# Kernel tuning notes

Hardware: AMD Instinct MI355X
Metric: run time of the kernel (lower is better)

## Reference

```python
import jax, jax.numpy as jnp
import numpy as np

PATCH = 7          # patch_size (stride fixed to 1, loop=False)
ALPHA = 0.01       # coherent_alpha


def extract_patches(x, p):
    # x: [1, C, T] -> [n, C*p], n = T - p + 1  (unfold over time, stride 1)
    b, c, t = x.shape
    n = t - p + 1
    idx = jnp.arange(n)[:, None] + jnp.arange(p)[None, :]   # [n, p]
    patches = x[0][:, idx]                                   # [C, n, p]
    return patches.transpose(1, 0, 2).reshape(n, c * p)      # [n, C*p]


def setup_inputs() -> dict:
    key = jax.random.key(0)
    kx, ky = jax.random.split(key)
    X = jax.random.normal(kx, (1, 72, 8192), dtype=jnp.float32)
    Y = jax.random.normal(ky, (1, 72, 8192), dtype=jnp.float32)
    return {"X": X, "Y": Y}


def reference(X, Y):
    p = PATCH
    b, c, t = X.shape
    d = c * p
    xp = extract_patches(X, p)                               # [n1, d]
    yp = extract_patches(Y, p)                               # [n2, d]
    # efficient_cdist: squared L2 distances, normalized by patch dim d
    dist = ((xp * xp).sum(1)[:, None] + (yp * yp).sum(1)[None, :]
            - 2.0 * (xp @ yp.T)) / d                         # [n1, n2]
    # coherent_alpha: bidirectional-similarity normalization by per-y-patch min
    norm_dist = dist / (ALPHA + dist.min(axis=0, keepdims=True))
    nnf = jnp.argmin(norm_dist, axis=1)                      # [n1] int
    dists = jnp.take_along_axis(dist, nnf[:, None], axis=1)[:, 0]
    # combine_patches: gather matched y patches, overlap-add (fold), normalize by counts
    matched = yp[nnf].reshape(-1, c, p)                      # [n1, C, p]
    n1 = matched.shape[0]
    idx = jnp.arange(n1)[:, None] + jnp.arange(p)[None, :]   # [n1, p] -> time index
    acc = jnp.zeros((c, t), X.dtype).at[:, idx].add(matched.transpose(1, 0, 2))
    cnt = jnp.zeros((t,), X.dtype).at[idx].add(jnp.ones((n1, p), X.dtype))
    blended = (acc / cnt)[None]                              # [1, C, T]
    return blended, dists.mean()
```

## Files before the change

### kernel.cpp

```cpp
#include <hip/hip_runtime.h>
#include <stdint.h>

#define TT 8192
#define CC 72
#define PP 7
#define NN (TT - PP + 1)
#define DD (CC * PP)

#define TI 122
#define SG 128
#define SPAD 132
#define NTILE ((NN + TI - 1) / TI)
#define NT2   (NTILE * NTILE)
#define GRID1 4608

#define STAGE_BYTES (CC * SG * 4)
#define SMEM_UNION  (2 * STAGE_BYTES)

#define TAIL_BYTES 196608

#define SROWS 4

constexpr float INV_D = 1.0f / (float)DD;
constexpr float ALPHA_C = 0.01f;
constexpr float QSCALE = 67108864.0f;

__global__ void prep_kernel(const float* __restrict__ X, const float* __restrict__ Y,
                            float* __restrict__ sx, float* __restrict__ sy,
                            unsigned* __restrict__ colmin,
                            unsigned long long* __restrict__ packed,
                            unsigned long long* __restrict__ qsum) {
    int i = blockIdx.x * 256 + threadIdx.x;
    if (blockIdx.y == 0) {
        if (i == 0) *qsum = 0ULL;
        if (i < TT) { colmin[i] = 0x7f800000u; packed[i] = ~0ULL; }
        if (i < NN) {
            float ax = 0.0f;
            for (int c = 0; c < CC; ++c) {
                const float* xr = X + c * TT + i;
#pragma unroll
                for (int k = 0; k < PP; ++k) { float v = xr[k]; ax += v * v; }
            }
            sx[i] = ax;
        }
    } else {
        if (i < NN) {
            float ay = 0.0f;
            for (int c = 0; c < CC; ++c) {
                const float* yr = Y + c * TT + i;
#pragma unroll
                for (int k = 0; k < PP; ++k) { float w = yr[k]; ay += w * w; }
            }
            sy[i] = ay;
        }
    }
}

__device__ __forceinline__ void tile_dots256(const float* __restrict__ X,
                                             const float* __restrict__ Y,
                                             int i0, int j0, char* smem,
                                             float dot[8][8]) {
    float (*Xs)[SG]   = (float (*)[SG])smem;
    float (*Ys)[SG]   = (float (*)[SG])(smem + STAGE_BYTES);
    float (*Sl)[SPAD] = (float (*)[SPAD])smem;
    const int tid = threadIdx.x;

    for (int idx = tid; idx < CC * SG / 2; idx += 256) {
        int c  = idx >> 6;
        int t2 = (idx & 63) * 2;
        int gx = i0 + t2, gy = j0 + t2;
        float2 xv, yv;
        if (gx + 1 < TT) xv = *(const float2*)(X + c * TT + gx);
        else { xv.x = X[c * TT + min(gx, TT - 1)]; xv.y = X[c * TT + min(gx + 1, TT - 1)]; }
        if (gy + 1 < TT) yv = *(const float2*)(Y + c * TT + gy);
        else { yv.x = Y[c * TT + min(gy, TT - 1)]; yv.y = Y[c * TT + min(gy + 1, TT - 1)]; }
        *(float2*)&Xs[c][t2] = xv;
        *(float2*)&Ys[c][t2] = yv;
    }
    __syncthreads();

    const int su = tid >> 4, sv = tid & 15;
    float s[8][8];
#pragma unroll
    for (int a = 0; a < 8; ++a)
#pragma unroll
        for (int b = 0; b < 8; ++b) s[a][b] = 0.0f;

#pragma unroll 4
    for (int c = 0; c < CC; ++c) {
        float xv[8], yv[8];
        *(float4*)&xv[0] = *(const float4*)&Xs[c][su * 8];
        *(float4*)&xv[4] = *(const float4*)&Xs[c][su * 8 + 4];
        *(float4*)&yv[0] = *(const float4*)&Ys[c][sv * 4];
        *(float4*)&yv[4] = *(const float4*)&Ys[c][64 + sv * 4];
#pragma unroll
        for (int a = 0; a < 8; ++a)
#pragma unroll
            for (int b = 0; b < 8; ++b)
                s[a][b] += xv[a] * yv[b];
    }
    __syncthreads();

#pragma unroll
    for (int a = 0; a < 8; ++a) {
        int row = su * 8 + a;
        int swz = ((row >> 3) & 3) << 2;
        *(float4*)&Sl[row][(sv * 4) ^ swz]      = make_float4(s[a][0], s[a][1], s[a][2], s[a][3]);
        *(float4*)&Sl[row][(64 + sv * 4) ^ swz] = make_float4(s[a][4], s[a][5], s[a][6], s[a][7]);
    }
    __syncthreads();

    const int ri = (tid >> 4) * 8, rj = (tid & 15) * 8;
#pragma unroll
    for (int a = 0; a < 8; ++a)
#pragma unroll
        for (int b = 0; b < 8; ++b) dot[a][b] = 0.0f;

#pragma unroll
    for (int r = 0; r < 14; ++r) {
        int row = ri + r;
        int swz = ((row >> 3) & 3) << 2;
        float f[14];
        *(float4*)&f[0]  = *(const float4*)&Sl[row][(rj)      ^ swz];
        *(float4*)&f[4]  = *(const float4*)&Sl[row][(rj + 4)  ^ swz];
        *(float4*)&f[8]  = *(const float4*)&Sl[row][(rj + 8)  ^ swz];
        *(float2*)&f[12] = *(const float2*)&Sl[row][(rj + 12) ^ swz];
#pragma unroll
        for (int a = 0; a < 8; ++a) {
            const int k = r - a;
            if (k >= 0 && k < PP) {
#pragma unroll
                for (int b = 0; b < 8; ++b)
                    dot[a][b] += f[b + k];
            }
        }
    }
}

__global__ __launch_bounds__(256) void pass1_k(
        const float* __restrict__ X, const float* __restrict__ Y,
        const float* __restrict__ sx, const float* __restrict__ sy,
        unsigned* __restrict__ colmin,
        float* __restrict__ distbuf, int storeTiles) {
    __shared__ __align__(16) char smem[SMEM_UNION + 1024];
    unsigned* cmin_s = (unsigned*)(smem + SMEM_UNION);
    const int tid = threadIdx.x;

    for (int tile = blockIdx.x; tile < NT2; tile += GRID1) {
        const int by = tile / NTILE, bx = tile - by * NTILE;
        const int i0 = by * TI;
        const int j0 = bx * TI;
        const bool store = (by < storeTiles);

        if (tid < 128) cmin_s[tid] = 0x7f800000u;

        float dot[8][8];
        tile_dots256(X, Y, i0, j0, smem, dot);

        const int ri = (tid >> 4) * 8, rj = (tid & 15) * 8;
        const int gj0 = j0 + rj;

        bool bv[8]; float syv[8];
#pragma unroll
        for (int b = 0; b < 8; ++b) {
            int lj = rj + b, gj = gj0 + b;
            bv[b] = (lj < TI && gj < NN);
            syv[b] = bv[b] ? sy[gj] : 0.0f;
        }
        const bool fullCols = (rj + 7 < TI) && (gj0 + 7 < NN);
        const bool al16 = ((gj0 & 3) == 0);

        float cm[8];
#pragma unroll
        for (int b = 0; b < 8; ++b) cm[b] = __uint_as_float(0x7f800000u);

#pragma unroll
        for (int a = 0; a < 8; ++a) {
            int li = ri + a, gi = i0 + li;
            if (li >= TI || gi >= NN) continue;
            float sxi = sx[gi];
            float d8[8];
#pragma unroll
            for (int b = 0; b < 8; ++b) {
                d8[b] = (sxi + syv[b] - 2.0f * dot[a][b]) * INV_D;
                if (bv[b]) cm[b] = fminf(cm[b], d8[b]);
            }
            if (store) {
                float* drow = distbuf + (size_t)gi * TT + gj0;
                if (fullCols) {
                    if (al16) {
                        *(float4*)&drow[0] = make_float4(d8[0], d8[1], d8[2], d8[3]);
                        *(float4*)&drow[4] = make_float4(d8[4], d8[5], d8[6], d8[7]);
                    } else {
                        *(float2*)&drow[0] = make_float2(d8[0], d8[1]);
                        *(float4*)&drow[2] = make_float4(d8[2], d8[3], d8[4], d8[5]);
                        *(float2*)&drow[6] = make_float2(d8[6], d8[7]);
                    }
                } else {
#pragma unroll
                    for (int b = 0; b < 8; ++b)
                        if (bv[b]) drow[b] = d8[b];
                }
            }
        }
#pragma unroll
        for (int b = 0; b < 8; ++b)
            if (bv[b]) atomicMin(&cmin_s[rj + b], __float_as_uint(cm[b]));
        __syncthreads();
        if (tid < TI) {
            int gj = j0 + tid;
            if (gj < NN) atomicMin(&colmin[gj], cmin_s[tid]);
        }
        __syncthreads();
    }
}

template<bool FULL>
__global__ __launch_bounds__(256) void pass2_stream_k(
        const float* __restrict__ distbuf, const unsigned* __restrict__ colmin,
        unsigned long long* __restrict__ packed,
        int* __restrict__ nnf, unsigned long long* __restrict__ qsum, int nrows) {
    const int i0 = blockIdx.x * SROWS;
    const float* row0 = distbuf + (size_t)i0 * TT;
    const float* cmf = (const float*)colmin;

    unsigned long long best[SROWS];
#pragma unroll
    for (int r = 0; r < SROWS; ++r) best[r] = ~0ULL;

    for (int jb = threadIdx.x * 8; jb < NN; jb += 2048) {
        float4 c4a = *(const float4*)(cmf + jb);
        float4 c4b = *(const float4*)(cmf + jb + 4);
        float acm[8];
#pragma unroll
        for (int e = 0; e < 8; ++e)
            acm[e] = ALPHA_C + ((e < 4) ? (&c4a.x)[e] : (&c4b.x)[e - 4]);
#pragma unroll
        for (int r = 0; r < SROWS; ++r) {
            const float* row = row0 + (size_t)r * TT;
            float4 d4a = *(const float4*)(row + jb);
            float4 d4b = *(const float4*)(row + jb + 4);
#pragma unroll
            for (int e = 0; e < 8; ++e) {
                int j = jb + e;
                if (j < NN) {
                    float d  = (e < 4) ? (&d4a.x)[e] : (&d4b.x)[e - 4];
                    float nd = d / acm[e];
                    unsigned long long pk =
                        ((unsigned long long)__float_as_uint(nd) << 32) | (unsigned)j;
                    best[r] = (pk < best[r]) ? pk : best[r];
                }
            }
        }
    }
#pragma unroll
    for (int r = 0; r < SROWS; ++r)
#pragma unroll
        for (int off = 32; off > 0; off >>= 1) {
            unsigned long long o = __shfl_down(best[r], off, 64);
            best[r] = (o < best[r]) ? o : best[r];
        }
    __shared__ unsigned long long wb[4][SROWS];
    int lane = threadIdx.x & 63, wid = threadIdx.x >> 6;
    if (lane == 0) {
#pragma unroll
        for (int r = 0; r < SROWS; ++r) wb[wid][r] = best[r];
    }
    __syncthreads();
    if (threadIdx.x < SROWS) {
        int r = threadIdx.x;
        int i = i0 + r;
        if (i < nrows) {
            unsigned long long b0 = wb[0][r];
            b0 = (wb[1][r] < b0) ? wb[1][r] : b0;
            b0 = (wb[2][r] < b0) ? wb[2][r] : b0;
            b0 = (wb[3][r] < b0) ? wb[3][r] : b0;
            if (FULL) {
                int j = (int)(b0 & 0xffffffffu);
                nnf[i] = j;
                float dval = distbuf[(size_t)i * TT + j];
                atomicAdd(qsum, (unsigned long long)(long long)(dval * QSCALE));
            } else {
                packed[i] = b0;
            }
        }
    }
}

__global__ __launch_bounds__(256) void pass2_k(
        const float* __restrict__ X, const float* __restrict__ Y,
        const float* __restrict__ sx, const float* __restrict__ sy,
        const unsigned* __restrict__ colmin,
        unsigned long long* __restrict__ packed, int itile_ofs) {
    __shared__ __align__(16) char smem[SMEM_UNION + 1024];
    unsigned long long* pmin_s = (unsigned long long*)(smem + SMEM_UNION);

    const int i0 = (itile_ofs + blockIdx.y) * TI;
    const int j0 = blockIdx.x * TI;
    const int tid = threadIdx.x;
    if (tid < TI) pmin_s[tid] = ~0ULL;

    float dot[8][8];
    tile_dots256(X, Y, i0, j0, smem, dot);

    const int ri = (tid >> 4) * 8, rj = (tid & 15) * 8;
    const int gj0 = j0 + rj;

    bool bv[8]; float syv[8], acm[8];
#pragma unroll
    for (int b = 0; b < 8; ++b) {
        int lj = rj + b, gj = gj0 + b;
        bv[b] = (lj < TI && gj < NN);
        syv[b] = bv[b] ? sy[gj] : 0.0f;
        acm[b] = bv[b] ? (ALPHA_C + __uint_as_float(colmin[gj])) : 1.0f;
    }

#pragma unroll
    for (int a = 0; a < 8; ++a) {
        int li = ri + a, gi = i0 + li;
        if (li >= TI || gi >= NN) continue;
        float sxi = sx[gi];
        unsigned long long best = ~0ULL;
#pragma unroll
        for (int b = 0; b < 8; ++b) {
            if (bv[b]) {
                float d  = (sxi + syv[b] - 2.0f * dot[a][b]) * INV_D;
                float nd = d / acm[b];
                unsigned long long pk =
                    ((unsigned long long)__float_as_uint(nd) << 32) | (unsigned)(gj0 + b);
                best = (pk < best) ? pk : best;
            }
        }
        atomicMin(&pmin_s[li], best);
    }
    __syncthreads();
    if (tid < TI) {
        int gi = i0 + tid;
        if (gi < NN) atomicMin(&packed[gi], pmin_s[tid]);
    }
}

__global__ void finalize_kernel(const float* __restrict__ X, const float* __restrict__ Y,
                                const float* __restrict__ sx, const float* __restrict__ sy,
                                const unsigned long long* __restrict__ packed,
                                int* __restrict__ nnf, unsigned long long* __restrict__ qsum) {
    int i = blockIdx.x * 256 + threadIdx.x;
    long long q = 0;
    if (i < NN) {
        int j = (int)(packed[i] & 0xffffffffu);
        nnf[i] = j;
        float dot = 0.0f;
        for (int c = 0; c < CC; ++c) {
            const float* xr = X + c * TT + i;
            const float* yr = Y + c * TT + j;
#pragma unroll
            for (int k = 0; k < PP; ++k) dot += xr[k] * yr[k];
        }
        float dval = (sx[i] + sy[j] - 2.0f * dot) * INV_D;
        q = (long long)(dval * QSCALE);
    }
    __shared__ long long red[256];
    red[threadIdx.x] = q;
    __syncthreads();
    for (int s = 128; s > 0; s >>= 1) {
        if (threadIdx.x < s) red[threadIdx.x] += red[threadIdx.x + s];
        __syncthreads();
    }
    if (threadIdx.x == 0) atomicAdd(qsum, (unsigned long long)red[0]);
}

__global__ void fold_kernel(const float* __restrict__ Y, const int* __restrict__ nnf,
                            const unsigned long long* __restrict__ qsum,
                            float* __restrict__ out) {
    int idx = blockIdx.x * 256 + threadIdx.x;
    if (idx < CC * TT) {
        int c = idx >> 13;
        int t = idx & (TT - 1);
        float acc = 0.0f;
        int cnt = 0;
#pragma unroll
        for (int k = 0; k < PP; ++k) {
            int i = t - k;
            if (i >= 0 && i < NN) {
                acc += Y[c * TT + nnf[i] + k];
                cnt++;
            }
        }
        out[idx] = acc / (float)cnt;
    }
    if (idx == 0) {
        double m = (double)*qsum * (1.0 / (double)QSCALE) / (double)NN;
        out[CC * TT] = (float)m;
    }
}

extern "C" void kernel_launch(void* const* d_in, const int* in_sizes, int n_in,
                              void* d_out, int out_size, void* d_ws, size_t ws_size,
                              hipStream_t stream) {
    const float* X = (const float*)d_in[0];
    const float* Y = (const float*)d_in[1];
    float* out = (float*)d_out;

    char* w = (char*)d_ws;
    size_t base = 0;
    if (ws_size > TAIL_BYTES) base = ((ws_size - TAIL_BYTES) / 32768) * 32768;
    unsigned long long* packed = (unsigned long long*)(w + base);
    unsigned*           colmin = (unsigned*)(w + base + 65536);
    float*              sx     = (float*)(w + base + 98304);
    float*              sy     = (float*)(w + base + 131072);
    int*                nnf    = (int*)(w + base + 163840);
    unsigned long long* qsum   = (unsigned long long*)(w + base + 196600);
    float*              distbuf = (float*)w;

    const long storeRows = (long)(base / ((size_t)TT * 4));
    int storeTiles = 0;
    for (int nT = 1; nT <= NTILE; ++nT) {
        long need = (long)nT * TI; if (need > NN) need = NN;
        if (need <= storeRows) storeTiles = nT; else break;
    }
    const int SR = (storeTiles * TI < NN) ? storeTiles * TI : NN;
    const bool full = (storeTiles >= NTILE);

    prep_kernel<<<dim3((TT + 255) / 256, 2), 256, 0, stream>>>(
        X, Y, sx, sy, colmin, packed, qsum);

    pass1_k<<<GRID1, 256, 0, stream>>>(X, Y, sx, sy, colmin, distbuf, storeTiles);

    if (full) {
        pass2_stream_k<true><<<(NN + SROWS - 1) / SROWS, 256, 0, stream>>>(
            distbuf, colmin, packed, nnf, qsum, NN);
    } else {
        if (SR > 0)
            pass2_stream_k<false><<<(SR + SROWS - 1) / SROWS, 256, 0, stream>>>(
                distbuf, colmin, packed, nnf, qsum, SR);
        if (storeTiles < NTILE) {
            dim3 grid2(NTILE, NTILE - storeTiles);
            pass2_k<<<grid2, 256, 0, stream>>>(X, Y, sx, sy, colmin, packed, storeTiles);
        }
        finalize_kernel<<<(NN + 255) / 256, 256, 0, stream>>>(X, Y, sx, sy, packed, nnf, qsum);
    }
    fold_kernel<<<(CC * TT + 255) / 256, 256, 0, stream>>>(Y, nnf, qsum, out);
}
```

Measured before the change: 290.7 us.

## Shrink pass1 tiles to 122x58 with channel-chunked staging for higher occupancy

After: 329.5 us. 1.13x slower.

```diff
diff --git a/kernel.cpp b/kernel.cpp
--- a/kernel.cpp
+++ b/kernel.cpp
@@ -7,18 +7,27 @@
 #define NN (TT - PP + 1)
 #define DD (CC * PP)
 
+#define SGI 128
+#define TII 122
+#define NTI 68
+#define SGJ 64
+#define TIJ 58
+#define NTJ 142
+#define NT2 (NTI * NTJ)
+#define SPADJ 68
+#define CH 36
+
+#define SL_BYTES 36608
+#define SMEM_TOT (SL_BYTES + 384)
+
 #define TI 122
 #define SG 128
 #define SPAD 132
-#define NTILE ((NN + TI - 1) / TI)
-#define NT2   (NTILE * NTILE)
-#define GRID1 4608
-
+#define NTILE 68
 #define STAGE_BYTES (CC * SG * 4)
 #define SMEM_UNION  (2 * STAGE_BYTES)
 
 #define TAIL_BYTES 196608
-
 #define SROWS 4
 
 constexpr float INV_D = 1.0f / (float)DD;
@@ -56,162 +65,156 @@
     }
 }
 
-__device__ __forceinline__ void tile_dots256(const float* __restrict__ X,
-                                             const float* __restrict__ Y,
-                                             int i0, int j0, char* smem,
-                                             float dot[8][8]) {
-    float (*Xs)[SG]   = (float (*)[SG])smem;
-    float (*Ys)[SG]   = (float (*)[SG])(smem + STAGE_BYTES);
-    float (*Sl)[SPAD] = (float (*)[SPAD])smem;
-    const int tid = threadIdx.x;
-
-    for (int idx = tid; idx < CC * SG / 2; idx += 256) {
-        int c  = idx >> 6;
-        int t2 = (idx & 63) * 2;
-        int gx = i0 + t2, gy = j0 + t2;
-        float2 xv, yv;
-        if (gx + 1 < TT) xv = *(const float2*)(X + c * TT + gx);
-        else { xv.x = X[c * TT + min(gx, TT - 1)]; xv.y = X[c * TT + min(gx + 1, TT - 1)]; }
-        if (gy + 1 < TT) yv = *(const float2*)(Y + c * TT + gy);
-        else { yv.x = Y[c * TT + min(gy, TT - 1)]; yv.y = Y[c * TT + min(gy + 1, TT - 1)]; }
-        *(float2*)&Xs[c][t2] = xv;
-        *(float2*)&Ys[c][t2] = yv;
-    }
-    __syncthreads();
-
-    const int su = tid >> 4, sv = tid & 15;
-    float s[8][8];
-#pragma unroll
-    for (int a = 0; a < 8; ++a)
-#pragma unroll
-        for (int b = 0; b < 8; ++b) s[a][b] = 0.0f;
-
-#pragma unroll 4
-    for (int c = 0; c < CC; ++c) {
-        float xv[8], yv[8];
-        *(float4*)&xv[0] = *(const float4*)&Xs[c][su * 8];
-        *(float4*)&xv[4] = *(const float4*)&Xs[c][su * 8 + 4];
-        *(float4*)&yv[0] = *(const float4*)&Ys[c][sv * 4];
-        *(float4*)&yv[4] = *(const float4*)&Ys[c][64 + sv * 4];
-#pragma unroll
-        for (int a = 0; a < 8; ++a)
-#pragma unroll
-            for (int b = 0; b < 8; ++b)
-                s[a][b] += xv[a] * yv[b];
-    }
-    __syncthreads();
-
-#pragma unroll
-    for (int a = 0; a < 8; ++a) {
-        int row = su * 8 + a;
-        int swz = ((row >> 3) & 3) << 2;
-        *(float4*)&Sl[row][(sv * 4) ^ swz]      = make_float4(s[a][0], s[a][1], s[a][2], s[a][3]);
-        *(float4*)&Sl[row][(64 + sv * 4) ^ swz] = make_float4(s[a][4], s[a][5], s[a][6], s[a][7]);
-    }
-    __syncthreads();
-
-    const int ri = (tid >> 4) * 8, rj = (tid & 15) * 8;
-#pragma unroll
-    for (int a = 0; a < 8; ++a)
-#pragma unroll
-        for (int b = 0; b < 8; ++b) dot[a][b] = 0.0f;
-
-#pragma unroll
-    for (int r = 0; r < 14; ++r) {
-        int row = ri + r;
-        int swz = ((row >> 3) & 3) << 2;
-        float f[14];
-        *(float4*)&f[0]  = *(const float4*)&Sl[row][(rj)      ^ swz];
-        *(float4*)&f[4]  = *(const float4*)&Sl[row][(rj + 4)  ^ swz];
-        *(float4*)&f[8]  = *(const float4*)&Sl[row][(rj + 8)  ^ swz];
-        *(float2*)&f[12] = *(const float2*)&Sl[row][(rj + 12) ^ swz];
-#pragma unroll
-        for (int a = 0; a < 8; ++a) {
-            const int k = r - a;
-            if (k >= 0 && k < PP) {
-#pragma unroll
-                for (int b = 0; b < 8; ++b)
-                    dot[a][b] += f[b + k];
-            }
-        }
-    }
-}
-
-__global__ __launch_bounds__(256) void pass1_k(
+__global__ __launch_bounds__(256, 4) void pass1_k(
         const float* __restrict__ X, const float* __restrict__ Y,
         const float* __restrict__ sx, const float* __restrict__ sy,
         unsigned* __restrict__ colmin,
         float* __restrict__ distbuf, int storeTiles) {
-    __shared__ __align__(16) char smem[SMEM_UNION + 1024];
-    unsigned* cmin_s = (unsigned*)(smem + SMEM_UNION);
+    __shared__ __align__(16) char smem[SMEM_TOT];
+    float (*Xs)[SGI]   = (float (*)[SGI])smem;
+    float (*Ys)[SGJ]   = (float (*)[SGJ])(smem + 18432);
+    float (*Sl)[SPADJ] = (float (*)[SPADJ])smem;
+    unsigned* cmin_s   = (unsigned*)(smem + SL_BYTES);
+
     const int tid = threadIdx.x;
-
-    for (int tile = blockIdx.x; tile < NT2; tile += GRID1) {
-        const int by = tile / NTILE, bx = tile - by * NTILE;
-        const int i0 = by * TI;
-        const int j0 = bx * TI;
-        const bool store = (by < storeTiles);
-
-        if (tid < 128) cmin_s[tid] = 0x7f800000u;
-
-        float dot[8][8];
-        tile_dots256(X, Y, i0, j0, smem, dot);
-
-        const int ri = (tid >> 4) * 8, rj = (tid & 15) * 8;
-        const int gj0 = j0 + rj;
-
-        bool bv[8]; float syv[8];
-#pragma unroll
-        for (int b = 0; b < 8; ++b) {
-            int lj = rj + b, gj = gj0 + b;
-            bv[b] = (lj < TI && gj < NN);
-            syv[b] = bv[b] ? sy[gj] : 0.0f;
-        }
-        const bool fullCols = (rj + 7 < TI) && (gj0 + 7 < NN);
-        const bool al16 = ((gj0 & 3) == 0);
-
-        float cm[8];
-#pragma unroll
-        for (int b = 0; b < 8; ++b) cm[b] = __uint_as_float(0x7f800000u);
-
+    const int su = tid >> 4, sv = tid & 15;
+    const int ri = su * 8, rj = sv * 4;
+
+    const int tile = blockIdx.x;
+    const int by = tile / NTJ, bx = tile - by * NTJ;
+    const int i0 = by * TII, j0 = bx * TIJ;
+    const bool store = (by < storeTiles);
+
+    if (tid < SGJ) cmin_s[tid] = 0x7f800000u;
+
+    float s[8][4];
+#pragma unroll
+    for (int a = 0; a < 8; ++a)
+#pragma unroll
+        for (int b = 0; b < 4; ++b) s[a][b] = 0.0f;
+
+    for (int h = 0; h < 2; ++h) {
+        for (int idx = tid; idx < 3456; idx += 256) {
+            if (idx < 2304) {
+                int cc = idx >> 6;
+                int t2 = (idx & 63) * 2;
+                int gx = i0 + t2;
+                const float* xp = X + (size_t)(CH * h + cc) * TT;
+                float2 xv;
+                if (gx + 1 < TT) xv = *(const float2*)(xp + gx);
+                else { xv.x = xp[min(gx, TT - 1)]; xv.y = xp[min(gx + 1, TT - 1)]; }
+                *(float2*)&Xs[cc][t2] = xv;
+            } else {
+                int iy = idx - 2304;
+                int cc = iy >> 5;
+                int t2 = (iy & 31) * 2;
+                int gy = j0 + t2;
+                const float* yp = Y + (size_t)(CH * h + cc) * TT;
+                float2 yv;
+                if (gy + 1 < TT) yv = *(const float2*)(yp + gy);
+                else { yv.x = yp[min(gy, TT - 1)]; yv.y = yp[min(gy + 1, TT - 1)]; }
+                *(float2*)&Ys[cc][t2] = yv;
+            }
+        }
+        __syncthreads();
+
+#pragma unroll 4
+        for (int cc = 0; cc < CH; ++cc) {
+            float xv[8], yv[4];
+            *(float4*)&xv[0] = *(const float4*)&Xs[cc][su * 8];
+            *(float4*)&xv[4] = *(const float4*)&Xs[cc][su * 8 + 4];
+            *(float4*)&yv[0] = *(const float4*)&Ys[cc][sv * 4];
+#pragma unroll
+            for (int a = 0; a < 8; ++a)
+#pragma unroll
+                for (int b = 0; b < 4; ++b)
+                    s[a][b] += xv[a] * yv[b];
+        }
+        __syncthreads();
+    }
+
+#pragma unroll
+    for (int a = 0; a < 8; ++a) {
+        int row = su * 8 + a;
+        int swz = ((row >> 3) & 3) << 2;
+        *(float4*)&Sl[row][(sv * 4) ^ swz] = make_float4(s[a][0], s[a][1], s[a][2], s[a][3]);
+    }
+    __syncthreads();
+
+    float dot[8][4];
+#pragma unroll
+    for (int a = 0; a < 8; ++a)
+#pragma unroll
+        for (int b = 0; b < 4; ++b) dot[a][b] = 0.0f;
+
+#pragma unroll
+    for (int r = 0; r < 14; ++r) {
+        int row = ri + r;
+        int swz = ((row >> 3) & 3) << 2;
+        float f[12];
+        *(float4*)&f[0] = *(const float4*)&Sl[row][(rj)     ^ swz];
+        *(float4*)&f[4] = *(const float4*)&Sl[row][(rj + 4) ^ swz];
+        *(float4*)&f[8] = *(const float4*)&Sl[row][(rj + 8) ^ swz];
 #pragma unroll
         for (int a = 0; a < 8; ++a) {
-            int li = ri + a, gi = i0 + li;
-            if (li >= TI || gi >= NN) continue;
-            float sxi = sx[gi];
-            float d8[8];
-#pragma unroll
-            for (int b = 0; b < 8; ++b) {
-                d8[b] = (sxi + syv[b] - 2.0f * dot[a][b]) * INV_D;
-                if (bv[b]) cm[b] = fminf(cm[b], d8[b]);
-            }
-            if (store) {
-                float* drow = distbuf + (size_t)gi * TT + gj0;
-                if (fullCols) {
-                    if (al16) {
-                        *(float4*)&drow[0] = make_float4(d8[0], d8[1], d8[2], d8[3]);
-                        *(float4*)&drow[4] = make_float4(d8[4], d8[5], d8[6], d8[7]);
-                    } else {
-                        *(float2*)&drow[0] = make_float2(d8[0], d8[1]);
-                        *(float4*)&drow[2] = make_float4(d8[2], d8[3], d8[4], d8[5]);
-                        *(float2*)&drow[6] = make_float2(d8[6], d8[7]);
-                    }
+            const int k = r - a;
+            if (k >= 0 && k < PP) {
+#pragma unroll
+                for (int b = 0; b < 4; ++b)
+                    dot[a][b] += f[b + k];
+            }
+        }
+    }
+
+    const int gj0 = j0 + rj;
+    bool bv[4]; float syv[4];
+#pragma unroll
+    for (int b = 0; b < 4; ++b) {
+        int lj = rj + b, gj = gj0 + b;
+        bv[b] = (lj < TIJ && gj < NN);
+        syv[b] = bv[b] ? sy[gj] : 0.0f;
+    }
+    const bool fullCols = (rj + 3 < TIJ) && (gj0 + 3 < NN);
+    const bool al16 = ((gj0 & 3) == 0);
+
+    float cm[4];
+#pragma unroll
+    for (int b = 0; b < 4; ++b) cm[b] = __uint_as_float(0x7f800000u);
+
+#pragma unroll
+    for (int a = 0; a < 8; ++a) {
+        int li = ri + a, gi = i0 + li;
+        if (li >= TII || gi >= NN) continue;
+        float sxi = sx[gi];
+        float d4[4];
+#pragma unroll
+        for (int b = 0; b < 4; ++b) {
+            d4[b] = (sxi + syv[b] - 2.0f * dot[a][b]) * INV_D;
+            if (bv[b]) cm[b] = fminf(cm[b], d4[b]);
+        }
+        if (store) {
+            float* drow = distbuf + (size_t)gi * TT + gj0;
+            if (fullCols) {
+                if (al16) {
+                    *(float4*)&drow[0] = make_float4(d4[0], d4[1], d4[2], d4[3]);
                 } else {
-#pragma unroll
-                    for (int b = 0; b < 8; ++b)
-                        if (bv[b]) drow[b] = d8[b];
+                    *(float2*)&drow[0] = make_float2(d4[0], d4[1]);
+                    *(float2*)&drow[2] = make_float2(d4[2], d4[3]);
                 }
-            }
-        }
-#pragma unroll
-        for (int b = 0; b < 8; ++b)
-            if (bv[b]) atomicMin(&cmin_s[rj + b], __float_as_uint(cm[b]));
-        __syncthreads();
-        if (tid < TI) {
-            int gj = j0 + tid;
-            if (gj < NN) atomicMin(&colmin[gj], cmin_s[tid]);
-        }
-        __syncthreads();
+            } else {
+#pragma unroll
+                for (int b = 0; b < 4; ++b)
+                    if (bv[b]) drow[b] = d4[b];
+            }
+        }
+    }
+#pragma unroll
+    for (int b = 0; b < 4; ++b)
+        if (bv[b]) atomicMin(&cmin_s[rj + b], __float_as_uint(cm[b]));
+    __syncthreads();
+    if (tid < TIJ) {
+        int gj = j0 + tid;
+        if (gj < NN) atomicMin(&colmin[gj], cmin_s[tid]);
     }
 }
 
@@ -287,6 +290,87 @@
     }
 }
 
+__device__ __forceinline__ void tile_dots256(const float* __restrict__ X,
+                                             const float* __restrict__ Y,
+                                             int i0, int j0, char* smem,
+                                             float dot[8][8]) {
+    float (*Xs)[SG]   = (float (*)[SG])smem;
+    float (*Ys)[SG]   = (float (*)[SG])(smem + STAGE_BYTES);
+    float (*Sl)[SPAD] = (float (*)[SPAD])smem;
+    const int tid = threadIdx.x;
+
+    for (int idx = tid; idx < CC * SG / 2; idx += 256) {
+        int c  = idx >> 6;
+        int t2 = (idx & 63) * 2;
+        int gx = i0 + t2, gy = j0 + t2;
+        float2 xv, yv;
+        if (gx + 1 < TT) xv = *(const float2*)(X + c * TT + gx);
+        else { xv.x = X[c * TT + min(gx, TT - 1)]; xv.y = X[c * TT + min(gx + 1, TT - 1)]; }
+        if (gy + 1 < TT) yv = *(const float2*)(Y + c * TT + gy);
+        else { yv.x = Y[c * TT + min(gy, TT - 1)]; yv.y = Y[c * TT + min(gy + 1, TT - 1)]; }
+        *(float2*)&Xs[c][t2] = xv;
+        *(float2*)&Ys[c][t2] = yv;
+    }
+    __syncthreads();
+
+    const int su = tid >> 4, sv = tid & 15;
+    float s[8][8];
+#pragma unroll
+    for (int a = 0; a < 8; ++a)
+#pragma unroll
+        for (int b = 0; b < 8; ++b) s[a][b] = 0.0f;
+
+#pragma unroll 4
+    for (int c = 0; c < CC; ++c) {
+        float xv[8], yv[8];
+        *(float4*)&xv[0] = *(const float4*)&Xs[c][su * 8];
+        *(float4*)&xv[4] = *(const float4*)&Xs[c][su * 8 + 4];
+        *(float4*)&yv[0] = *(const float4*)&Ys[c][sv * 4];
+        *(float4*)&yv[4] = *(const float4*)&Ys[c][64 + sv * 4];
+#pragma unroll
+        for (int a = 0; a < 8; ++a)
+#pragma unroll
+            for (int b = 0; b < 8; ++b)
+                s[a][b] += xv[a] * yv[b];
+    }
+    __syncthreads();
+
+#pragma unroll
+    for (int a = 0; a < 8; ++a) {
+        int row = su * 8 + a;
+        int swz = ((row >> 3) & 3) << 2;
+        *(float4*)&Sl[row][(sv * 4) ^ swz]      = make_float4(s[a][0], s[a][1], s[a][2], s[a][3]);
+        *(float4*)&Sl[row][(64 + sv * 4) ^ swz] = make_float4(s[a][4], s[a][5], s[a][6], s[a][7]);
+    }
+    __syncthreads();
+
+    const int ri = (tid >> 4) * 8, rj = (tid & 15) * 8;
+#pragma unroll
+    for (int a = 0; a < 8; ++a)
+#pragma unroll
+        for (int b = 0; b < 8; ++b) dot[a][b] = 0.0f;
+
+#pragma unroll
+    for (int r = 0; r < 14; ++r) {
+        int row = ri + r;
+        int swz = ((row >> 3) & 3) << 2;
+        float f[14];
+        *(float4*)&f[0]  = *(const float4*)&Sl[row][(rj)      ^ swz];
+        *(float4*)&f[4]  = *(const float4*)&Sl[row][(rj + 4)  ^ swz];
+        *(float4*)&f[8]  = *(const float4*)&Sl[row][(rj + 8)  ^ swz];
+        *(float2*)&f[12] = *(const float2*)&Sl[row][(rj + 12) ^ swz];
+#pragma unroll
+        for (int a = 0; a < 8; ++a) {
+            const int k = r - a;
+            if (k >= 0 && k < PP) {
+#pragma unroll
+                for (int b = 0; b < 8; ++b)
+                    dot[a][b] += f[b + k];
+            }
+        }
+    }
+}
+
 __global__ __launch_bounds__(256) void pass2_k(
         const float* __restrict__ X, const float* __restrict__ Y,
         const float* __restrict__ sx, const float* __restrict__ sy,
@@ -414,17 +498,17 @@
 
     const long storeRows = (long)(base / ((size_t)TT * 4));
     int storeTiles = 0;
-    for (int nT = 1; nT <= NTILE; ++nT) {
-        long need = (long)nT * TI; if (need > NN) need = NN;
+    for (int nT = 1; nT <= NTI; ++nT) {
+        long need = (long)nT * TII; if (need > NN) need = NN;
         if (need <= storeRows) storeTiles = nT; else break;
     }
-    const int SR = (storeTiles * TI < NN) ? storeTiles * TI : NN;
-    const bool full = (storeTiles >= NTILE);
+    const int SR = (storeTiles * TII < NN) ? storeTiles * TII : NN;
+    const bool full = (storeTiles >= NTI);
 
     prep_kernel<<<dim3((TT + 255) / 256, 2), 256, 0, stream>>>(
         X, Y, sx, sy, colmin, packed, qsum);
 
-    pass1_k<<<GRID1, 256, 0, stream>>>(X, Y, sx, sy, colmin, distbuf, storeTiles);
+    pass1_k<<<NT2, 256, 0, stream>>>(X, Y, sx, sy, colmin, distbuf, storeTiles);
 
     if (full) {
         pass2_stream_k<true><<<(NN + SROWS - 1) / SROWS, 256, 0, stream>>>(
@@ -433,7 +517,7 @@
         if (SR > 0)
             pass2_stream_k<false><<<(SR + SROWS - 1) / SROWS, 256, 0, stream>>>(
                 distbuf, colmin, packed, nnf, qsum, SR);
-        if (storeTiles < NTILE) {
+        if (storeTiles < NTI) {
             dim3 grid2(NTILE, NTILE - storeTiles);
             pass2_k<<<grid2, 256, 0, stream>>>(X, Y, sx, sy, colmin, packed, storeTiles);
         }
```
